# Kernel tuning notes

Measured on AMD Instinct MI355X. Metric: run time of the kernel, lower is better.

Reference implementation:

```python
import jax, jax.numpy as jnp
import numpy as np

N = 100000      # nodes
E = 1600000     # edges (avg degree 16)
DIN = 128
DOUT = 128


def setup_inputs() -> dict:
    key = jax.random.key(0)
    k1, k2, k3, k4 = jax.random.split(key, 4)
    x = jax.random.normal(k1, (N, DIN), dtype=jnp.float32)
    # destination rows: ensure every node appears at least once so the
    # bincount-based degree normalization never divides by zero
    row = jnp.concatenate([jnp.arange(N, dtype=jnp.int32),
                           jax.random.randint(k2, (E - N,), 0, N, dtype=jnp.int32)])
    col = jax.random.randint(k3, (E,), 0, N, dtype=jnp.int32)
    edge_index = jnp.stack([row, col])  # [2, E]
    # reset_parameters: weight ~ U(-stdv, stdv), stdv = 6/sqrt(in+out); bias = 0
    stdv = 6.0 / np.sqrt(DIN + DOUT)
    W = jax.random.uniform(k4, (DIN, DOUT), dtype=jnp.float32, minval=-stdv, maxval=stdv)
    bias = jnp.zeros((DOUT,), dtype=jnp.float32)
    alpha = jnp.full((DOUT,), 0.25, dtype=jnp.float32)  # PReLU per-channel init
    return {"x": x, "W": W, "bias": bias, "alpha": alpha,
            "edge_index": edge_index, "activation": 0}


def reference(x, W, bias, alpha, edge_index, activation):
    n = x.shape[0]
    support = x @ W                                   # [N, DOUT]
    row, col = edge_index[0], edge_index[1]
    # output.index_add_(0, row, support[col])
    agg = jax.ops.segment_sum(support[col], row, num_segments=n)   # [N, DOUT]
    # degree = bincount(row, minlength=N)
    deg = jax.ops.segment_sum(jnp.ones((row.shape[0],), support.dtype), row,
                              num_segments=n)[:, None]             # [N, 1]
    out = agg / deg
    d10 = support.shape[1] // 10
    h = jnp.concatenate([out[:, :d10], support[:, d10:]], axis=1) + bias
    # PReLU with per-channel alpha
    return jnp.where(h >= 0, h, alpha * h)
```

## Files before the change

### kernel.cpp

```cpp
#include <hip/hip_runtime.h>

#define DIM 128
#define D10 12

typedef __attribute__((ext_vector_type(8))) short bf16x8;
typedef __attribute__((ext_vector_type(4))) float f32x4;

__device__ __forceinline__ void fma4(float4& a, float s, const float4& w) {
    a.x = fmaf(s, w.x, a.x);
    a.y = fmaf(s, w.y, a.y);
    a.z = fmaf(s, w.z, a.z);
    a.w = fmaf(s, w.w, a.w);
}

__device__ __forceinline__ unsigned short f2bf(float f) {
    union { float f; unsigned int u; } v; v.f = f;
    unsigned int u = v.u;
    unsigned int r = (u + 0x7FFFu + ((u >> 16) & 1u)) >> 16;
    return (unsigned short)r;
}

__device__ __forceinline__ float bf2f(unsigned int hi16) {
    union { unsigned int u; float f; } v; v.u = hi16 << 16;
    return v.f;
}

__device__ __forceinline__ void atomPkAddBf16(unsigned int* p, unsigned int v) {
    unsigned long long a = (unsigned long long)p;
    asm volatile("global_atomic_pk_add_bf16 %0, %1, off" :: "v"(a), "v"(v) : "memory");
}

__device__ __forceinline__ void atomAddF32(float* p, float v) {
    unsafeAtomicAdd(p, v);
}


__global__ void k_wt(const float* __restrict__ W, unsigned short* __restrict__ Wt) {
    int i = blockIdx.x * 256 + threadIdx.x;
    if (i >= DIM * DIM) return;
    int k = i >> 7, nn = i & 127;
    Wt[nn * DIM + k] = f2bf(W[i]);
}


__global__ __launch_bounds__(256) void k_s12(const float4* __restrict__ xv,
                                             const float4* __restrict__ Wv,
                                             unsigned int* __restrict__ s12b, int n) {
    __shared__ float4 xsf[64 * 33];
    __shared__ float4 w12[128 * 3];

    int tid = threadIdx.x;
    int rowbase = blockIdx.x * 64;

    for (int i = tid; i < 128 * 3; i += 256) {
        int k = i / 3, q = i - k * 3;
        w12[i] = Wv[k * 32 + q];
    }
    for (int i = tid; i < 64 * 32; i += 256) {
        int r = rowbase + (i >> 5);
        float4 v; v.x = v.y = v.z = v.w = 0.f;
        if (r < n) v = xv[(size_t)r * 32 + (i & 31)];
        xsf[(i >> 5) * 33 + (i & 31)] = v;
    }
    __syncthreads();

    if (tid < 192) {
        int lrow = tid / 3;
        int q = tid - lrow * 3;
        const float4* xr = &xsf[lrow * 33];
        float4 acc; acc.x = acc.y = acc.z = acc.w = 0.f;
#pragma unroll 4
        for (int k4 = 0; k4 < 32; ++k4) {
            float4 v = xr[k4];
            float4 w0 = w12[(k4 * 4 + 0) * 3 + q];
            float4 w1 = w12[(k4 * 4 + 1) * 3 + q];
            float4 w2 = w12[(k4 * 4 + 2) * 3 + q];
            float4 w3 = w12[(k4 * 4 + 3) * 3 + q];
            fma4(acc, v.x, w0); fma4(acc, v.y, w1);
            fma4(acc, v.z, w2); fma4(acc, v.w, w3);
        }
        int grow = rowbase + lrow;
        if (grow < n) {
            unsigned int p0 = (unsigned int)f2bf(acc.x) | ((unsigned int)f2bf(acc.y) << 16);
            unsigned int p1 = (unsigned int)f2bf(acc.z) | ((unsigned int)f2bf(acc.w) << 16);
            s12b[(size_t)grow * 6 + 2 * q]     = p0;
            s12b[(size_t)grow * 6 + 2 * q + 1] = p1;
        }
    }
}


__global__ __launch_bounds__(256) void k_fat(
    const float4* __restrict__ xv, float* __restrict__ out,
    const uint4* __restrict__ Wtv,
    const float* __restrict__ bias, const float* __restrict__ alpha,
    const unsigned int* __restrict__ s12b,
    const int* __restrict__ row, const int* __restrict__ col,
    unsigned int* __restrict__ agg,
    int gemmBlocks, long long aggTotal, int n)
{
    __shared__ alignas(16) char xs[16 * 1024];

    if ((int)blockIdx.x >= gemmBlocks) {
        int aggBlocks = gridDim.x - gemmBlocks;
        long long i = (long long)((int)blockIdx.x - gemmBlocks) * 256 + threadIdx.x;
        long long stride = (long long)aggBlocks * 256;
        for (long long g = i; g < aggTotal; g += stride) {
            int e = (int)(g >> 3), l = (int)(g & 7);
            if (l < 7) {
                int r = row[e];
                unsigned int v = (l < 6) ? s12b[(size_t)col[e] * 6 + l]
                                         : 0x00003F80u;
                atomPkAddBf16(&agg[(size_t)r * 8 + l], v);
            }
        }
        return;
    }

    int tid = threadIdx.x;
    int rowbase = blockIdx.x * 64;

#pragma unroll
    for (int ii = 0; ii < 8; ++ii) {
        int i = tid + ii * 256;
        int lr = i >> 5, c4 = i & 31;
        int r = rowbase + lr;
        float4 v; v.x = v.y = v.z = v.w = 0.f;
        if (r < n) v = xv[(size_t)r * 32 + c4];
        uint2 p;
        p.x = (unsigned int)f2bf(v.x) | ((unsigned int)f2bf(v.y) << 16);
        p.y = (unsigned int)f2bf(v.z) | ((unsigned int)f2bf(v.w) << 16);
        int byte = (lr * 256 + c4 * 8) ^ ((lr & 7) << 4);
        *reinterpret_cast<uint2*>(xs + byte) = p;
    }
    __syncthreads();

    int wv = tid >> 6;
    int lane = tid & 63;
    int lr0 = wv * 16;
    int arow = lr0 + (lane & 15);
    int kgrp = (lane >> 4) * 8;

    const char* Wb = reinterpret_cast<const char*>(Wtv);

    f32x4 acc[8];
#pragma unroll
    for (int t = 0; t < 8; ++t) acc[t] = (f32x4){0.f, 0.f, 0.f, 0.f};

#pragma unroll
    for (int kb = 0; kb < 4; ++kb) {
        int koff = kb * 32 + kgrp;
        int abyte = (arow * 256 + koff * 2) ^ ((arow & 7) << 4);
        bf16x8 a = *reinterpret_cast<const bf16x8*>(xs + abyte);
#pragma unroll
        for (int t = 0; t < 8; ++t) {
            int c = t * 16 + (lane & 15);
            bf16x8 b = *reinterpret_cast<const bf16x8*>(Wb + (c * DIM + koff) * 2);
            acc[t] = __builtin_amdgcn_mfma_f32_16x16x32_bf16(a, b, acc[t], 0, 0, 0);
        }
    }

    int colbase = lane & 15;
    int rgrp = (lane >> 4) * 4;
    float bi[8], al[8];
#pragma unroll
    for (int t = 0; t < 8; ++t) {
        int c = t * 16 + colbase;
        bi[t] = bias[c];
        al[t] = alpha[c];
    }
#pragma unroll
    for (int j = 0; j < 4; ++j) {
        int r = rowbase + lr0 + rgrp + j;
        if (r >= n) continue;
#pragma unroll
        for (int t = 0; t < 8; ++t) {
            int c = t * 16 + colbase;
            if (t == 0 && colbase < D10) continue;
            float h = acc[t][j];
            h += bi[t];
            h = h >= 0.f ? h : al[t] * h;
            out[(size_t)r * DIM + c] = h;
        }
    }
}


__global__ void k_epi12(const uint4* __restrict__ aggv, const float* __restrict__ bias,
                        const float* __restrict__ alpha, float* __restrict__ out, int n) {
    int r = blockIdx.x * blockDim.x + threadIdx.x;
    if (r >= n) return;
    uint4 a0 = aggv[(size_t)r * 2];
    uint4 a1 = aggv[(size_t)r * 2 + 1];
    float dg = bf2f(a1.z & 0xFFFFu);
    float invd = 1.f / (dg >= 1.f ? dg : 1.f);
    unsigned int s[6] = {a0.x, a0.y, a0.z, a0.w, a1.x, a1.y};
    float h[12];
#pragma unroll
    for (int q = 0; q < 6; ++q) {
        h[2 * q]     = bf2f(s[q] & 0xFFFFu) * invd + bias[2 * q];
        h[2 * q + 1] = bf2f(s[q] >> 16)     * invd + bias[2 * q + 1];
    }
#pragma unroll
    for (int c = 0; c < 12; ++c) {
        float v = h[c];
        h[c] = v >= 0.f ? v : alpha[c] * v;
    }
    float4* o = reinterpret_cast<float4*>(out + (size_t)r * DIM);
    o[0] = make_float4(h[0], h[1], h[2], h[3]);
    o[1] = make_float4(h[4], h[5], h[6], h[7]);
    o[2] = make_float4(h[8], h[9], h[10], h[11]);
}


__global__ void k_count_deg(const int* __restrict__ row, int E, int* __restrict__ deg) {
    int i = blockIdx.x * blockDim.x + threadIdx.x;
    int stride = gridDim.x * blockDim.x;
    for (; i < E; i += stride) atomicAdd(&deg[row[i]], 1);
}

__global__ void k_edge_atomic(const float4* __restrict__ xv, const int* __restrict__ row,
                              const int* __restrict__ col, int E, float* __restrict__ out) {
    int i = blockIdx.x * blockDim.x + threadIdx.x;
    int stride = gridDim.x * blockDim.x;
    int total = E * 32;
    for (; i < total; i += stride) {
        int e = i >> 5, lane = i & 31;
        int r = row[e], c = col[e];
        float4 v = xv[(size_t)c * 32 + lane];
        float* dst = out + (size_t)r * DIM + lane * 4;
        atomAddF32(dst + 0, v.x);
        atomAddF32(dst + 1, v.y);
        atomAddF32(dst + 2, v.z);
        atomAddF32(dst + 3, v.w);
    }
}

__global__ __launch_bounds__(256) void k_final_legacy(const float4* __restrict__ xv,
                                                      float4* __restrict__ outv,
                                                      const float4* __restrict__ Wv,
                                                      const float4* __restrict__ biasv,
                                                      const float4* __restrict__ alphav,
                                                      const int* __restrict__ deg, int n) {
    __shared__ float4 Ws4[DIM * 32];
    __shared__ float4 vs4[2][32 * 32];

    int tid = threadIdx.x;
    int rowbase = blockIdx.x * 32;
    if (rowbase >= n) return;

    for (int i = tid; i < DIM * 32; i += 256) Ws4[i] = Wv[i];
    for (int i = tid; i < 32 * 32; i += 256) {
        int r = rowbase + (i >> 5);
        if (r < n) {
            vs4[0][i] = outv[(size_t)r * 32 + (i & 31)];
            vs4[1][i] = xv[(size_t)r * 32 + (i & 31)];
        }
    }
    __syncthreads();

    int tx = tid & 31;
    int ty = tid >> 5;
    int r0 = ty * 4;
    const float4* V = (tx < (D10 / 4)) ? vs4[0] : vs4[1];

    float4 acc[4];
#pragma unroll
    for (int r = 0; r < 4; r++) { acc[r].x = acc[r].y = acc[r].z = acc[r].w = 0.f; }

#pragma unroll 8
    for (int k4 = 0; k4 < 32; k4++) {
        float4 w0 = Ws4[(k4 * 4 + 0) * 32 + tx];
        float4 w1 = Ws4[(k4 * 4 + 1) * 32 + tx];
        float4 w2 = Ws4[(k4 * 4 + 2) * 32 + tx];
        float4 w3 = Ws4[(k4 * 4 + 3) * 32 + tx];
#pragma unroll
        for (int r = 0; r < 4; r++) {
            float4 v = V[(r0 + r) * 32 + k4];
            fma4(acc[r], v.x, w0); fma4(acc[r], v.y, w1);
            fma4(acc[r], v.z, w2); fma4(acc[r], v.w, w3);
        }
    }

    float4 b4 = biasv[tx];
    float4 a4 = alphav[tx];
#pragma unroll
    for (int r = 0; r < 4; r++) {
        int row = rowbase + r0 + r;
        if (row >= n) continue;
        float4 h = acc[r];
        if (tx < (D10 / 4)) {
            int d = deg[row];
            float invd = 1.0f / (float)(d > 0 ? d : 1);
            h.x *= invd; h.y *= invd; h.z *= invd; h.w *= invd;
        }
        h.x += b4.x; h.y += b4.y; h.z += b4.z; h.w += b4.w;
        h.x = h.x >= 0.f ? h.x : a4.x * h.x;
        h.y = h.y >= 0.f ? h.y : a4.y * h.y;
        h.z = h.z >= 0.f ? h.z : a4.z * h.z;
        h.w = h.w >= 0.f ? h.w : a4.w * h.w;
        outv[(size_t)row * 32 + tx] = h;
    }
}


extern "C" void kernel_launch(void* const* d_in, const int* in_sizes, int n_in,
                              void* d_out, int out_size, void* d_ws, size_t ws_size,
                              hipStream_t stream) {
    const float* x     = (const float*)d_in[0];
    const float* W     = (const float*)d_in[1];
    const float* bias  = (const float*)d_in[2];
    const float* alpha = (const float*)d_in[3];
    const int*   ei    = (const int*)d_in[4];

    int N = in_sizes[0] / DIM;
    int E = in_sizes[4] / 2;
    const int* row = ei;
    const int* col = ei + E;
    float* out = (float*)d_out;

    int gemmBlocks = (N + 63) / 64;
    int aggBlocks  = 2048;
    size_t wt_bytes = (size_t)DIM * DIM * 2;

    size_t need_A = wt_bytes + (size_t)(6 + 8) * N * 4;
    size_t need_E = (size_t)N * 4;

    if (ws_size >= need_A) {
        unsigned short* Wt   = (unsigned short*)d_ws;
        unsigned int* s12b   = (unsigned int*)((char*)d_ws + wt_bytes);
        unsigned int* agg    = s12b + (size_t)6 * N;

        hipMemsetAsync(agg, 0, (size_t)8 * N * sizeof(unsigned int), stream);
        k_wt<<<(DIM * DIM + 255) / 256, 256, 0, stream>>>(W, Wt);
        k_s12<<<gemmBlocks, 256, 0, stream>>>((const float4*)x, (const float4*)W,
                                              s12b, N);
        long long aggTotal = (long long)E * 8;
        k_fat<<<gemmBlocks + aggBlocks, 256, 0, stream>>>(
            (const float4*)x, out, (const uint4*)Wt, bias, alpha,
            s12b, row, col, agg, gemmBlocks, aggTotal, N);
        k_epi12<<<(N + 255) / 256, 256, 0, stream>>>((const uint4*)agg, bias, alpha, out, N);
    } else if (ws_size >= need_E) {
        int* deg = (int*)d_ws;
        hipMemsetAsync(out, 0, (size_t)N * DIM * sizeof(float), stream);
        hipMemsetAsync(deg, 0, (size_t)N * sizeof(int), stream);
        k_count_deg<<<2048, 256, 0, stream>>>(row, E, deg);
        k_edge_atomic<<<4096, 256, 0, stream>>>((const float4*)x, row, col, E, out);
        k_final_legacy<<<(N + 31) / 32, 256, 0, stream>>>((const float4*)x, (float4*)out,
                                                          (const float4*)W, (const float4*)bias,
                                                          (const float4*)alpha, deg, N);
    }
}
```

Baseline: 146.2 us.

## Fuse weight transpose into s12 kernel, seed aggregation, stage W in LDS

Moves the bf16 weight transpose into the k_s12 kernel and drops the separate memset. A new init kernel seeds each aggregation row from its self-loop edge, using the fact that the first N edges have row==index, and the atomic loop then skips those edges. The fused kernel now puts the 256 aggregation blocks first in the grid and stages the transposed weight in swizzled LDS (48KB) instead of reading it from global memory. The seeding relies on the test's edge layout, since it checks row[e]==e at runtime for the first N edges, and the larger LDS footprint may reduce occupancy. It also depends on the Wt write in k_s12 finishing before k_fat reads it, which stream ordering guarantees.

```diff
diff --git a/kernel.cpp b/kernel.cpp
--- a/kernel.cpp
+++ b/kernel.cpp
@@ -2,6 +2,7 @@
 
 #define DIM 128
 #define D10 12
+#define ABLK 256
 
 typedef __attribute__((ext_vector_type(8))) short bf16x8;
 typedef __attribute__((ext_vector_type(4))) float f32x4;
@@ -35,22 +36,22 @@
 }
 
 
-__global__ void k_wt(const float* __restrict__ W, unsigned short* __restrict__ Wt) {
-    int i = blockIdx.x * 256 + threadIdx.x;
-    if (i >= DIM * DIM) return;
-    int k = i >> 7, nn = i & 127;
-    Wt[nn * DIM + k] = f2bf(W[i]);
-}
-
-
 __global__ __launch_bounds__(256) void k_s12(const float4* __restrict__ xv,
+                                             const float* __restrict__ W,
                                              const float4* __restrict__ Wv,
+                                             unsigned short* __restrict__ Wt,
                                              unsigned int* __restrict__ s12b, int n) {
     __shared__ float4 xsf[64 * 33];
     __shared__ float4 w12[128 * 3];
 
     int tid = threadIdx.x;
     int rowbase = blockIdx.x * 64;
+
+    int gwt = blockIdx.x * 256 + tid;
+    if (gwt < DIM * DIM) {
+        int k = gwt >> 7, nn = gwt & 127;
+        Wt[nn * DIM + k] = f2bf(W[gwt]);
+    }
 
     for (int i = tid; i < 128 * 3; i += 256) {
         int k = i / 3, q = i - k * 3;
@@ -90,6 +91,26 @@
 }
 
 
+__global__ void k_init(const unsigned int* __restrict__ s12b,
+                       const int* __restrict__ row, const int* __restrict__ col,
+                       unsigned int* __restrict__ agg, int n) {
+    int e = blockIdx.x * 256 + threadIdx.x;
+    if (e >= n) return;
+    uint4 a0 = make_uint4(0u, 0u, 0u, 0u);
+    uint4 a1 = make_uint4(0u, 0u, 0u, 0u);
+    if (row[e] == e) {
+        int c = col[e];
+        const unsigned int* s = s12b + (size_t)c * 6;
+        a0.x = s[0]; a0.y = s[1]; a0.z = s[2]; a0.w = s[3];
+        a1.x = s[4]; a1.y = s[5];
+        a1.z = 0x00003F80u;
+    }
+    uint4* dst = reinterpret_cast<uint4*>(agg + (size_t)e * 8);
+    dst[0] = a0;
+    dst[1] = a1;
+}
+
+
 __global__ __launch_bounds__(256) void k_fat(
     const float4* __restrict__ xv, float* __restrict__ out,
     const uint4* __restrict__ Wtv,
@@ -97,18 +118,18 @@
     const unsigned int* __restrict__ s12b,
     const int* __restrict__ row, const int* __restrict__ col,
     unsigned int* __restrict__ agg,
-    int gemmBlocks, long long aggTotal, int n)
+    long long aggTotal, int n)
 {
-    __shared__ alignas(16) char xs[16 * 1024];
-
-    if ((int)blockIdx.x >= gemmBlocks) {
-        int aggBlocks = gridDim.x - gemmBlocks;
-        long long i = (long long)((int)blockIdx.x - gemmBlocks) * 256 + threadIdx.x;
-        long long stride = (long long)aggBlocks * 256;
+    __shared__ alignas(16) char lds[48 * 1024];
+
+    if ((int)blockIdx.x < ABLK) {
+        long long i = (long long)blockIdx.x * 256 + threadIdx.x;
+        long long stride = (long long)ABLK * 256;
         for (long long g = i; g < aggTotal; g += stride) {
             int e = (int)(g >> 3), l = (int)(g & 7);
             if (l < 7) {
                 int r = row[e];
+                if (e < n && r == e) continue;
                 unsigned int v = (l < 6) ? s12b[(size_t)col[e] * 6 + l]
                                          : 0x00003F80u;
                 atomPkAddBf16(&agg[(size_t)r * 8 + l], v);
@@ -117,9 +138,20 @@
         return;
     }
 
+    char* xs  = lds;
+    char* wsm = lds + 16384;
+
     int tid = threadIdx.x;
-    int rowbase = blockIdx.x * 64;
-
+    int rowbase = ((int)blockIdx.x - ABLK) * 64;
+
+#pragma unroll
+    for (int ii = 0; ii < 8; ++ii) {
+        int i = tid + ii * 256;
+        int nn = i >> 4, kq = i & 15;
+        uint4 v = Wtv[nn * 16 + kq];
+        int byte = (nn * 256 + kq * 16) ^ ((nn & 7) << 4);
+        *reinterpret_cast<uint4*>(wsm + byte) = v;
+    }
 #pragma unroll
     for (int ii = 0; ii < 8; ++ii) {
         int i = tid + ii * 256;
@@ -141,8 +173,6 @@
     int arow = lr0 + (lane & 15);
     int kgrp = (lane >> 4) * 8;
 
-    const char* Wb = reinterpret_cast<const char*>(Wtv);
-
     f32x4 acc[8];
 #pragma unroll
     for (int t = 0; t < 8; ++t) acc[t] = (f32x4){0.f, 0.f, 0.f, 0.f};
@@ -155,7 +185,8 @@
 #pragma unroll
         for (int t = 0; t < 8; ++t) {
             int c = t * 16 + (lane & 15);
-            bf16x8 b = *reinterpret_cast<const bf16x8*>(Wb + (c * DIM + koff) * 2);
+            int bbyte = (c * 256 + koff * 2) ^ ((c & 7) << 4);
+            bf16x8 b = *reinterpret_cast<const bf16x8*>(wsm + bbyte);
             acc[t] = __builtin_amdgcn_mfma_f32_16x16x32_bf16(a, b, acc[t], 0, 0, 0);
         }
     }
@@ -320,7 +351,6 @@
     float* out = (float*)d_out;
 
     int gemmBlocks = (N + 63) / 64;
-    int aggBlocks  = 2048;
     size_t wt_bytes = (size_t)DIM * DIM * 2;
 
     size_t need_A = wt_bytes + (size_t)(6 + 8) * N * 4;
@@ -331,14 +361,13 @@
         unsigned int* s12b   = (unsigned int*)((char*)d_ws + wt_bytes);
         unsigned int* agg    = s12b + (size_t)6 * N;
 
-        hipMemsetAsync(agg, 0, (size_t)8 * N * sizeof(unsigned int), stream);
-        k_wt<<<(DIM * DIM + 255) / 256, 256, 0, stream>>>(W, Wt);
-        k_s12<<<gemmBlocks, 256, 0, stream>>>((const float4*)x, (const float4*)W,
-                                              s12b, N);
+        k_s12<<<gemmBlocks, 256, 0, stream>>>((const float4*)x, W, (const float4*)W,
+                                              Wt, s12b, N);
+        k_init<<<(N + 255) / 256, 256, 0, stream>>>(s12b, row, col, agg, N);
         long long aggTotal = (long long)E * 8;
-        k_fat<<<gemmBlocks + aggBlocks, 256, 0, stream>>>(
+        k_fat<<<ABLK + gemmBlocks, 256, 0, stream>>>(
             (const float4*)x, out, (const uint4*)Wt, bias, alpha,
-            s12b, row, col, agg, gemmBlocks, aggTotal, N);
+            s12b, row, col, agg, aggTotal, N);
         k_epi12<<<(N + 255) / 256, 256, 0, stream>>>((const uint4*)agg, bias, alpha, out, N);
     } else if (ws_size >= need_E) {
         int* deg = (int*)d_ws;
```

New measurement: 223.9 us. 1.53x slower.
